# Performance work log

Hardware: AMD Instinct MI355X
Metric: run time of the kernel (lower is better)

Reference implementation:

```python
import jax, jax.numpy as jnp
import numpy as np
import math

B, TSRC, TTGT, DM, DI, H = 2, 2048, 2048, 1024, 1024, 16
DH = DI // H
LN_EPS = 1e-5


def setup_inputs() -> dict:
    key = jax.random.key(0)
    ks = iter(jax.random.split(key, 40))
    def p(*shape):
        return jax.random.normal(next(ks), shape, jnp.float32) * 0.02
    inp = {
        "enc_out_vecs": jax.random.normal(next(ks), (B, TSRC, DM), jnp.float32),
        "output_vecs": jax.random.normal(next(ks), (B, TTGT, DM), jnp.float32),
    }
    for tag in ("dd", "ed"):
        inp["Wq_" + tag] = p(DM, DI); inp["bq_" + tag] = jnp.zeros((DI,), jnp.float32)
        inp["Wk_" + tag] = p(DM, DI); inp["bk_" + tag] = jnp.zeros((DI,), jnp.float32)
        inp["Wv_" + tag] = p(DM, DI); inp["bv_" + tag] = jnp.zeros((DI,), jnp.float32)
        inp["Wo_" + tag] = p(DI, DM); inp["bo_" + tag] = jnp.zeros((DM,), jnp.float32)
        inp["W1_" + tag] = p(DM, 2 * DM); inp["b1_" + tag] = jnp.zeros((2 * DM,), jnp.float32)
        inp["W2_" + tag] = p(2 * DM, DM); inp["b2_" + tag] = jnp.zeros((DM,), jnp.float32)
        inp["g1_" + tag] = jnp.ones((DM,), jnp.float32); inp["be1_" + tag] = jnp.zeros((DM,), jnp.float32)
        inp["g2_" + tag] = jnp.ones((DM,), jnp.float32); inp["be2_" + tag] = jnp.zeros((DM,), jnp.float32)
    return inp


def _ln(x, g, b):
    m = jnp.mean(x, axis=-1, keepdims=True)
    v = jnp.var(x, axis=-1, keepdims=True)
    return (x - m) * jax.lax.rsqrt(v + LN_EPS) * g + b


def _mha(xq, xkv, Wq, bq, Wk, bk, Wv, bv, causal):
    Bb, Tq, _ = xq.shape
    Tk = xkv.shape[1]
    q = (xq @ Wq + bq).reshape(Bb, Tq, H, DH)
    k = (xkv @ Wk + bk).reshape(Bb, Tk, H, DH)
    v = (xkv @ Wv + bv).reshape(Bb, Tk, H, DH)
    s = jnp.einsum("bqhd,bkhd->bhqk", q, k) / math.sqrt(DH)
    if causal:
        mask = jnp.where(jnp.arange(Tk)[None, :] > jnp.arange(Tq)[:, None], -jnp.inf, 0.0)
        s = s + mask
    w = jax.nn.softmax(s, axis=-1)
    return jnp.einsum("bhqk,bkhd->bqhd", w, v).reshape(Bb, Tq, H * DH)


def reference(enc_out_vecs, output_vecs,
              Wq_dd, bq_dd, Wk_dd, bk_dd, Wv_dd, bv_dd, Wo_dd, bo_dd,
              W1_dd, b1_dd, W2_dd, b2_dd, g1_dd, be1_dd, g2_dd, be2_dd,
              Wq_ed, bq_ed, Wk_ed, bk_ed, Wv_ed, bv_ed, Wo_ed, bo_ed,
              W1_ed, b1_ed, W2_ed, b2_ed, g1_ed, be1_ed, g2_ed, be2_ed):
    # masked self-attention over decoder inputs
    x = output_vecs
    a = _mha(x, x, Wq_dd, bq_dd, Wk_dd, bk_dd, Wv_dd, bv_dd, causal=True)
    x = _ln(a @ Wo_dd + bo_dd + x, g1_dd, be1_dd)
    x = _ln(x + jax.nn.relu(x @ W1_dd + b1_dd) @ W2_dd + b2_dd, g2_dd, be2_dd)
    # cross attention against encoder outputs
    a = _mha(x, enc_out_vecs, Wq_ed, bq_ed, Wk_ed, bk_ed, Wv_ed, bv_ed, causal=False)
    x = _ln(a @ Wo_ed + bo_ed + x, g1_ed, be1_ed)
    x = _ln(jax.nn.relu(x @ W1_ed + b1_ed) @ W2_ed + b2_ed + x, g2_ed, be2_ed)
    return x
```

## Files before the change

kernel.cpp:

```cpp
#include <hip/hip_runtime.h>
#include <stdint.h>

#define DEV __device__ __forceinline__
typedef unsigned short u16;
typedef __attribute__((ext_vector_type(8))) short bf16x8;
typedef __attribute__((ext_vector_type(4))) float f32x4;

#define AS1 __attribute__((address_space(1)))
#define AS3 __attribute__((address_space(3)))
#define WAITVM0 asm volatile("s_waitcnt vmcnt(0)" ::: "memory")
#define QSCALE 0.18033688011112042f

DEV u16 f2bf(float f) {
  union { float f; uint32_t u; } x; x.f = f;
  uint32_t r = x.u + 0x7fffu + ((x.u >> 16) & 1u);
  return (u16)(r >> 16);
}

DEV uint32_t cvt_pk_bf16(float a, float b) {
  uint32_t r;
  asm("v_cvt_pk_bf16_f32 %0, %1, %2" : "=v"(r) : "v"(a), "v"(b));
  return r;
}

__global__ __launch_bounds__(256) void k_cvt2(const float* __restrict__ a, const float* __restrict__ bsrc,
                                              u16* __restrict__ oa, u16* __restrict__ ob, int n4) {
  int i = blockIdx.x * blockDim.x + threadIdx.x;
  const float* s;
  u16* o;
  int k;
  if (i < n4) { s = a; o = oa; k = i; }
  else        { s = bsrc; o = ob; k = i - n4; }
  float4 v = reinterpret_cast<const float4*>(s)[k];
  reinterpret_cast<ushort4*>(o)[k] = make_ushort4(f2bf(v.x), f2bf(v.y), f2bf(v.z), f2bf(v.w));
}

struct WTJob { const float* W; u16* WT; int K, M, msh, start; };
struct WTJobs { WTJob j[12]; };

__global__ void k_wT_all(WTJobs jobs) {
  __shared__ float tile[32][33];
  int b = blockIdx.x;
  int i = 0;
#pragma unroll
  for (int t = 1; t < 12; ++t)
    if (b >= jobs.j[t].start) i = t;
  const WTJob J = jobs.j[i];
  int rel = b - J.start;
  int m0 = (rel & ((1 << J.msh) - 1)) << 5;
  int k0 = (rel >> J.msh) << 5;
  int tx = threadIdx.x, ty = threadIdx.y;
#pragma unroll
  for (int q = 0; q < 4; ++q)
    tile[ty + q * 8][tx] = J.W[(size_t)(k0 + ty + q * 8) * J.M + m0 + tx];
  __syncthreads();
#pragma unroll
  for (int q = 0; q < 4; ++q)
    J.WT[(size_t)(m0 + ty + q * 8) * J.K + k0 + tx] = f2bf(tile[tx][ty + q * 8]);
}

template<int R>
DEV void stage_tile(const u16* __restrict__ g, int strideElems, u16* lds, int tid, int wv) {
#pragma unroll
  for (int t = 0; t < R / 32; ++t) {
    int idx = t * 256 + tid;
    int row = idx >> 3;
    int b = (idx & 7) << 4;
    int sb = b ^ ((row & 7) << 4);
    const char* src = (const char*)g + (size_t)row * strideElems * 2 + sb;
    char* dst = (char*)lds + (size_t)(t * 256 + wv * 64) * 16;
    __builtin_amdgcn_global_load_lds((const AS1 void*)src, (AS3 void*)dst, 16, 0, 0);
  }
}

DEV bf16x8 lds_frag(const u16* lds, int row, int kel) {
  int off = row * 128 + ((kel * 2) ^ ((row & 7) << 4));
  return *(const bf16x8*)((const char*)lds + off);
}

template<int MODE>
__global__ __launch_bounds__(256) void k_gemm(const u16* __restrict__ A, int lda,
                                              const u16* __restrict__ BT,
                                              const float* __restrict__ bias,
                                              void* __restrict__ C, int ldc, int K) {
  __shared__ __align__(16) u16 A_lds[2][128 * 64];
  __shared__ __align__(16) u16 B_lds[2][128 * 64];
  const int tid = threadIdx.x, lane = tid & 63, wv = tid >> 6;
  const int wm = wv >> 1, wn = wv & 1;
  const int bm0 = blockIdx.y * 128, bn0 = blockIdx.x * 128;
  const int lr = lane & 15, lk = (lane >> 4) * 8, r0 = (lane >> 4) * 4;

  f32x4 acc[4][4];
#pragma unroll
  for (int i = 0; i < 4; ++i)
#pragma unroll
    for (int j = 0; j < 4; ++j) acc[i][j] = f32x4{0.f, 0.f, 0.f, 0.f};

  stage_tile<128>(A + (size_t)bm0 * lda, lda, A_lds[0], tid, wv);
  stage_tile<128>(BT + (size_t)bn0 * K, K, B_lds[0], tid, wv);
  WAITVM0;
  __builtin_amdgcn_s_barrier();

  int cur = 0;
  for (int k0 = 0; k0 < K; k0 += 64) {
    if (k0 + 64 < K) {
      stage_tile<128>(A + (size_t)bm0 * lda + k0 + 64, lda, A_lds[cur ^ 1], tid, wv);
      stage_tile<128>(BT + (size_t)bn0 * K + k0 + 64, K, B_lds[cur ^ 1], tid, wv);
    }
#pragma unroll
    for (int kk = 0; kk < 2; ++kk) {
      bf16x8 af[4], bfr[4];
#pragma unroll
      for (int i = 0; i < 4; ++i) af[i] = lds_frag(A_lds[cur], wm * 64 + i * 16 + lr, kk * 32 + lk);
#pragma unroll
      for (int j = 0; j < 4; ++j) bfr[j] = lds_frag(B_lds[cur], wn * 64 + j * 16 + lr, kk * 32 + lk);
#pragma unroll
      for (int i = 0; i < 4; ++i)
#pragma unroll
        for (int j = 0; j < 4; ++j)
          acc[i][j] = __builtin_amdgcn_mfma_f32_16x16x32_bf16(af[i], bfr[j], acc[i][j], 0, 0, 0);
    }
    WAITVM0;
    __builtin_amdgcn_s_barrier();
    cur ^= 1;
  }

#pragma unroll
  for (int j = 0; j < 4; ++j) {
    int col = bn0 + wn * 64 + j * 16 + lr;
    float bv = bias[col];
#pragma unroll
    for (int i = 0; i < 4; ++i) {
      int rowb = bm0 + wm * 64 + i * 16 + r0;
      if constexpr (MODE == 0) {
#pragma unroll
        for (int r = 0; r < 4; ++r)
          ((float*)C)[(size_t)(rowb + r) * ldc + col] = acc[i][j][r] + bv;
      } else {
#pragma unroll
        for (int r = 0; r < 4; ++r) {
          float v = fmaxf(acc[i][j][r] + bv, 0.f);
          ((u16*)C)[(size_t)(rowb + r) * ldc + col] = f2bf(v);
        }
      }
    }
  }
}

__global__ __launch_bounds__(256) void k_qkv(const u16* __restrict__ Aq, const u16* __restrict__ Akv,
                                             const u16* __restrict__ BT,
                                             const float* __restrict__ bq, const float* __restrict__ bk,
                                             const float* __restrict__ bv,
                                             u16* __restrict__ Qb, u16* __restrict__ Kb,
                                             u16* __restrict__ Vt, int K) {
  __shared__ __align__(16) u16 A_lds[2][128 * 64];
  __shared__ __align__(16) u16 B_lds[2][128 * 64];
  const int tid = threadIdx.x, lane = tid & 63, wv = tid >> 6;
  const int wm = wv >> 1, wn = wv & 1;
  const int bm0 = blockIdx.y * 128, bn0 = blockIdx.x * 128;
  const int seg = bn0 >> 10;
  const u16* A = (seg == 0) ? Aq : Akv;
  const int lr = lane & 15, lk = (lane >> 4) * 8, r0 = (lane >> 4) * 4;

  f32x4 acc[4][4];
#pragma unroll
  for (int i = 0; i < 4; ++i)
#pragma unroll
    for (int j = 0; j < 4; ++j) acc[i][j] = f32x4{0.f, 0.f, 0.f, 0.f};

  stage_tile<128>(A + (size_t)bm0 * K, K, A_lds[0], tid, wv);
  stage_tile<128>(BT + (size_t)bn0 * K, K, B_lds[0], tid, wv);
  WAITVM0;
  __builtin_amdgcn_s_barrier();

  int cur = 0;
  for (int k0 = 0; k0 < K; k0 += 64) {
    if (k0 + 64 < K) {
      stage_tile<128>(A + (size_t)bm0 * K + k0 + 64, K, A_lds[cur ^ 1], tid, wv);
      stage_tile<128>(BT + (size_t)bn0 * K + k0 + 64, K, B_lds[cur ^ 1], tid, wv);
    }
#pragma unroll
    for (int kk = 0; kk < 2; ++kk) {
      bf16x8 af[4], bfr[4];
#pragma unroll
      for (int i = 0; i < 4; ++i) af[i] = lds_frag(A_lds[cur], wm * 64 + i * 16 + lr, kk * 32 + lk);
#pragma unroll
      for (int j = 0; j < 4; ++j) bfr[j] = lds_frag(B_lds[cur], wn * 64 + j * 16 + lr, kk * 32 + lk);
#pragma unroll
      for (int i = 0; i < 4; ++i)
#pragma unroll
        for (int j = 0; j < 4; ++j)
          acc[i][j] = __builtin_amdgcn_mfma_f32_16x16x32_bf16(af[i], bfr[j], acc[i][j], 0, 0, 0);
    }
    WAITVM0;
    __builtin_amdgcn_s_barrier();
    cur ^= 1;
  }

#pragma unroll
  for (int j = 0; j < 4; ++j) {
    int col = bn0 + wn * 64 + j * 16 + lr;
    int cl = col & 1023;
#pragma unroll
    for (int i = 0; i < 4; ++i) {
      int rowb = bm0 + wm * 64 + i * 16 + r0;
      if (seg == 0) {
        float bb = bq[cl];
#pragma unroll
        for (int r = 0; r < 4; ++r)
          Qb[(size_t)(rowb + r) * 1024 + cl] = f2bf((acc[i][j][r] + bb) * QSCALE);
      } else if (seg == 1) {
        float bb = bk[cl];
#pragma unroll
        for (int r = 0; r < 4; ++r)
          Kb[(size_t)(rowb + r) * 1024 + cl] = f2bf(acc[i][j][r] + bb);
      } else {
        float bb = bv[cl];
        int bidx = rowb >> 11, t = rowb & 2047;
        ushort4 o = make_ushort4(f2bf(acc[i][j][0] + bb), f2bf(acc[i][j][1] + bb),
                                 f2bf(acc[i][j][2] + bb), f2bf(acc[i][j][3] + bb));
        *reinterpret_cast<ushort4*>(&Vt[((size_t)bidx * 1024 + cl) * 2048 + t]) = o;
      }
    }
  }
}

__global__ __launch_bounds__(256) void k_ln(const float* __restrict__ Rm, const float* __restrict__ X,
                                            const float* __restrict__ g, const float* __restrict__ be,
                                            float* __restrict__ Y, u16* __restrict__ Yb) {
  int row = blockIdx.x;
  size_t base4 = (size_t)row * 256;
  int t = threadIdx.x;
  float4 a = reinterpret_cast<const float4*>(Rm)[base4 + t];
  float4 x = reinterpret_cast<const float4*>(X)[base4 + t];
  float v0 = a.x + x.x, v1 = a.y + x.y, v2 = a.z + x.z, v3 = a.w + x.w;
  float s = v0 + v1 + v2 + v3;
  float ss = v0 * v0 + v1 * v1 + v2 * v2 + v3 * v3;
#pragma unroll
  for (int m = 1; m < 64; m <<= 1) { s += __shfl_xor(s, m); ss += __shfl_xor(ss, m); }
  __shared__ float red[8];
  int wv = t >> 6;
  if ((t & 63) == 0) { red[wv] = s; red[4 + wv] = ss; }
  __syncthreads();
  s = red[0] + red[1] + red[2] + red[3];
  ss = red[4] + red[5] + red[6] + red[7];
  float mean = s * (1.f / 1024.f);
  float var = ss * (1.f / 1024.f) - mean * mean;
  float rstd = rsqrtf(var + 1e-5f);
  float4 gv = reinterpret_cast<const float4*>(g)[t];
  float4 bv = reinterpret_cast<const float4*>(be)[t];
  float o0 = (v0 - mean) * rstd * gv.x + bv.x;
  float o1 = (v1 - mean) * rstd * gv.y + bv.y;
  float o2 = (v2 - mean) * rstd * gv.z + bv.z;
  float o3 = (v3 - mean) * rstd * gv.w + bv.w;
  reinterpret_cast<float4*>(Y)[base4 + t] = make_float4(o0, o1, o2, o3);
  if (Yb) {
    ushort4 ob = make_ushort4(f2bf(o0), f2bf(o1), f2bf(o2), f2bf(o3));
    reinterpret_cast<ushort4*>(Yb)[base4 + t] = ob;
  }
}

template<bool CAUSAL>
__global__ __launch_bounds__(256) void k_attn(const u16* __restrict__ Q, const u16* __restrict__ Kg,
                                              const u16* __restrict__ Vt, u16* __restrict__ O, int T) {
  __shared__ __align__(16) u16 K_lds[2][64 * 64];
  __shared__ __align__(16) u16 V_lds[2][64 * 64];
  __shared__ __align__(16) u16 p_lds[4][16 * 64];
  const int tid = threadIdx.x, lane = tid & 63, wv = tid >> 6;
  const int h = blockIdx.y, b = blockIdx.z;
  const int qx = CAUSAL ? (gridDim.x - 1 - blockIdx.x) : blockIdx.x;
  const int q0 = qx * 64;
  const int qw = q0 + wv * 16;
  const int lq = lane & 15, g = lane >> 4;
  const int swz = (lq & 7) << 4;
  const int fb0 = lq * 128 + ((g * 16) ^ swz);
  const int fb1 = lq * 128 + ((g * 16 + 64) ^ swz);
  const size_t qkbase = ((size_t)b * T) * 1024 + h * 64;
  const size_t vbase = ((size_t)b * 1024 + h * 64) * T;

  bf16x8 aq0, aq1;
  {
    const u16* qp = Q + qkbase + (size_t)(qw + lq) * 1024 + g * 8;
    aq0 = *reinterpret_cast<const bf16x8*>(qp);
    aq1 = *reinterpret_cast<const bf16x8*>(qp + 32);
  }

  const int srow = tid >> 3;
  const int ssb = ((tid & 7) << 4) ^ ((srow & 7) << 4);
  const char* ksrc = (const char*)(Kg + qkbase) + (size_t)srow * 2048 + ssb;
  const char* vsrc = (const char*)(Vt + vbase) + (size_t)srow * ((size_t)T * 2) + ssb;
  const int vstep2 = T * 64;
  const uint32_t doff = (uint32_t)((tid & 192) << 4);

  auto stage = [&](const char* kp, const char* vp, int buf) {
    char* kd = (char*)K_lds[buf] + doff;
    char* vd = (char*)V_lds[buf] + doff;
    __builtin_amdgcn_global_load_lds((const AS1 void*)kp, (AS3 void*)kd, 16, 0, 0);
    __builtin_amdgcn_global_load_lds((const AS1 void*)(kp + 65536), (AS3 void*)(kd + 4096), 16, 0, 0);
    __builtin_amdgcn_global_load_lds((const AS1 void*)vp, (AS3 void*)vd, 16, 0, 0);
    __builtin_amdgcn_global_load_lds((const AS1 void*)(vp + vstep2), (AS3 void*)(vd + 4096), 16, 0, 0);
  };

  f32x4 acc[4];
#pragma unroll
  for (int j = 0; j < 4; ++j) acc[j] = f32x4{0.f, 0.f, 0.f, 0.f};
  float lsum = 0.f;

  const int nt = CAUSAL ? (qx + 1) : (T >> 6);

  stage(ksrc, vsrc, 0);
  WAITVM0;
  __builtin_amdgcn_s_barrier();
  ksrc += 131072;
  vsrc += 128;

  char* pw = (char*)p_lds[wv];
  int cur = 0;
  for (int it = 0; it < nt; ++it) {
    const int kv0 = it << 6;
    if (it + 1 < nt) {
      stage(ksrc, vsrc, cur ^ 1);
      ksrc += 131072;
      vsrc += 128;
    }
    const char* kb = (const char*)K_lds[cur];
    const char* vb = (const char*)V_lds[cur];
    f32x4 st[4];
    __builtin_amdgcn_s_setprio(1);
#pragma unroll
    for (int j = 0; j < 4; ++j) {
      bf16x8 bk0 = *reinterpret_cast<const bf16x8*>(kb + fb0 + j * 2048);
      bf16x8 bk1 = *reinterpret_cast<const bf16x8*>(kb + fb1 + j * 2048);
      f32x4 t0 = f32x4{0.f, 0.f, 0.f, 0.f};
      t0 = __builtin_amdgcn_mfma_f32_16x16x32_bf16(bk0, aq0, t0, 0, 0, 0);
      t0 = __builtin_amdgcn_mfma_f32_16x16x32_bf16(bk1, aq1, t0, 0, 0, 0);
      st[j] = t0;
    }
    __builtin_amdgcn_s_setprio(0);
    uint32_t pk[8];
    if (CAUSAL && it == nt - 1) {
      const int qrow = qw + lq;
#pragma unroll
      for (int j = 0; j < 4; ++j) {
        float p0 = __builtin_exp2f(st[j][0]);
        float p1 = __builtin_exp2f(st[j][1]);
        float p2 = __builtin_exp2f(st[j][2]);
        float p3 = __builtin_exp2f(st[j][3]);
        int kvb = kv0 + j * 16 + g * 4;
        p0 = (kvb > qrow) ? 0.f : p0;
        p1 = (kvb + 1 > qrow) ? 0.f : p1;
        p2 = (kvb + 2 > qrow) ? 0.f : p2;
        p3 = (kvb + 3 > qrow) ? 0.f : p3;
        lsum += (p0 + p1) + (p2 + p3);
        pk[2 * j] = cvt_pk_bf16(p0, p1);
        pk[2 * j + 1] = cvt_pk_bf16(p2, p3);
      }
    } else {
#pragma unroll
      for (int j = 0; j < 4; ++j) {
        float p0 = __builtin_exp2f(st[j][0]);
        float p1 = __builtin_exp2f(st[j][1]);
        float p2 = __builtin_exp2f(st[j][2]);
        float p3 = __builtin_exp2f(st[j][3]);
        lsum += (p0 + p1) + (p2 + p3);
        pk[2 * j] = cvt_pk_bf16(p0, p1);
        pk[2 * j + 1] = cvt_pk_bf16(p2, p3);
      }
    }
#pragma unroll
    for (int j = 0; j < 4; ++j)
      *reinterpret_cast<uint2*>(pw + lq * 128 + ((j * 32 + g * 8) ^ swz)) =
          make_uint2(pk[2 * j], pk[2 * j + 1]);
    bf16x8 pf0 = *reinterpret_cast<const bf16x8*>(pw + fb0);
    bf16x8 pf1 = *reinterpret_cast<const bf16x8*>(pw + fb1);
    __builtin_amdgcn_s_setprio(1);
#pragma unroll
    for (int j2 = 0; j2 < 4; ++j2) {
      bf16x8 v0 = *reinterpret_cast<const bf16x8*>(vb + fb0 + j2 * 2048);
      bf16x8 v1 = *reinterpret_cast<const bf16x8*>(vb + fb1 + j2 * 2048);
      acc[j2] = __builtin_amdgcn_mfma_f32_16x16x32_bf16(v0, pf0, acc[j2], 0, 0, 0);
      acc[j2] = __builtin_amdgcn_mfma_f32_16x16x32_bf16(v1, pf1, acc[j2], 0, 0, 0);
    }
    __builtin_amdgcn_s_setprio(0);
    WAITVM0;
    __builtin_amdgcn_s_barrier();
    cur ^= 1;
  }

  lsum += __shfl_xor(lsum, 16);
  lsum += __shfl_xor(lsum, 32);
  float inv = 1.f / lsum;
  size_t rb = qkbase + (size_t)(qw + lq) * 1024;
#pragma unroll
  for (int j2 = 0; j2 < 4; ++j2) {
    ushort4 o = make_ushort4(f2bf(acc[j2][0] * inv), f2bf(acc[j2][1] * inv),
                             f2bf(acc[j2][2] * inv), f2bf(acc[j2][3] * inv));
    *reinterpret_cast<ushort4*>(&O[rb + j2 * 16 + g * 4]) = o;
  }
}

extern "C" void kernel_launch(void* const* d_in, const int* in_sizes, int n_in,
                              void* d_out, int out_size, void* d_ws, size_t ws_size,
                              hipStream_t stream) {
  const int T = 2048;
  const float* enc = (const float*)d_in[0];
  const float* outv = (const float*)d_in[1];
  auto F = [&](int i) { return (const float*)d_in[i]; };

  size_t off = 0;
  auto alloc = [&](size_t bytes) {
    void* p = (char*)d_ws + off;
    off += (bytes + 255) & ~(size_t)255;
    return p;
  };

  const int tdK[12] = {1024, 1024, 1024, 1024, 1024, 2048, 1024, 1024, 1024, 1024, 1024, 2048};
  const int tdM[12] = {1024, 1024, 1024, 1024, 2048, 1024, 1024, 1024, 1024, 1024, 2048, 1024};
  const int tdIdx[12] = {2, 4, 6, 8, 10, 12, 18, 20, 22, 24, 26, 28};
  u16* WT_[12];
  for (int i = 0; i < 12; ++i) WT_[i] = (u16*)alloc((size_t)tdK[i] * tdM[i] * 2);

  u16* Xb0 = (u16*)alloc(4096ull * 1024 * 2);
  u16* Eb = (u16*)alloc(4096ull * 1024 * 2);
  u16* Qb = (u16*)alloc(4096ull * 1024 * 2);
  u16* Kb = (u16*)alloc(4096ull * 1024 * 2);
  u16* Vt = (u16*)alloc(4096ull * 1024 * 2);
  u16* Ab = (u16*)alloc(4096ull * 1024 * 2);
  u16* Hb = (u16*)alloc(4096ull * 2048 * 2);
  u16* Xbc = (u16*)alloc(4096ull * 1024 * 2);
  float* Rf = (float*)alloc(4096ull * 1024 * 4);
  float* Xfa = (float*)alloc(4096ull * 1024 * 4);
  float* Xfb = (float*)alloc(4096ull * 1024 * 4);

  k_cvt2<<<8192, 256, 0, stream>>>(outv, enc, Xb0, Eb, 4096 * 1024 / 4);

  WTJobs jobs;
  int start = 0;
  for (int i = 0; i < 12; ++i) {
    int msh = (tdM[i] == 2048) ? 6 : 5;
    jobs.j[i] = {F(tdIdx[i]), WT_[i], tdK[i], tdM[i], msh, start};
    start += (tdM[i] >> 5) * (tdK[i] >> 5);
  }
  k_wT_all<<<start, dim3(32, 8), 0, stream>>>(jobs);

  dim3 gq(24, 32);
  dim3 g1k(8, 32);
  dim3 g2k(16, 32);
  dim3 ga(32, 16, 2);

  k_qkv<<<gq, 256, 0, stream>>>(Xb0, Xb0, WT_[0], F(3), F(5), F(7), Qb, Kb, Vt, 1024);
  k_attn<true><<<ga, 256, 0, stream>>>(Qb, Kb, Vt, Ab, T);
  k_gemm<0><<<g1k, 256, 0, stream>>>(Ab, 1024, WT_[3], F(9), Rf, 1024, 1024);
  k_ln<<<4096, 256, 0, stream>>>(Rf, outv, F(14), F(15), Xfa, Xbc);
  k_gemm<2><<<g2k, 256, 0, stream>>>(Xbc, 1024, WT_[4], F(11), Hb, 2048, 1024);
  k_gemm<0><<<g1k, 256, 0, stream>>>(Hb, 2048, WT_[5], F(13), Rf, 1024, 2048);
  k_ln<<<4096, 256, 0, stream>>>(Rf, Xfa, F(16), F(17), Xfb, Xbc);

  k_qkv<<<gq, 256, 0, stream>>>(Xbc, Eb, WT_[6], F(19), F(21), F(23), Qb, Kb, Vt, 1024);
  k_attn<false><<<ga, 256, 0, stream>>>(Qb, Kb, Vt, Ab, T);
  k_gemm<0><<<g1k, 256, 0, stream>>>(Ab, 1024, WT_[9], F(25), Rf, 1024, 1024);
  k_ln<<<4096, 256, 0, stream>>>(Rf, Xfb, F(30), F(31), Xfa, Xbc);
  k_gemm<2><<<g2k, 256, 0, stream>>>(Xbc, 1024, WT_[10], F(27), Hb, 2048, 1024);
  k_gemm<0><<<g1k, 256, 0, stream>>>(Hb, 2048, WT_[11], F(29), Rf, 1024, 2048);
  k_ln<<<4096, 256, 0, stream>>>(Rf, Xfa, F(32), F(33), (float*)d_out, (u16*)nullptr);
}
```

Before: 486.1 us.

## Split causal attention KV range across two blocks, shrink GEMM N-tiles, swizzle blocks

Causal self-attention now splits each query tile's KV range into two halves handled by separate blocks. Each block writes unnormalised fp32 partial outputs and row sums, and a new merge kernel combines them into bf16. This balances the triangular workload and doubles the block count. The N=1024 GEMMs and the QKV projection use narrower 64-column tiles for more workgroups, and all GEMMs use a grid swizzle for L2 locality. The cost is extra partial-result traffic, one more launch, and lower per-block arithmetic intensity.

Measured after the change: 452.1 us. 7.0% less time.

```diff
diff --git a/kernel.cpp b/kernel.cpp
--- a/kernel.cpp
+++ b/kernel.cpp
@@ -78,26 +78,31 @@
   return *(const bf16x8*)((const char*)lds + off);
 }
 
-template<int MODE>
+template<int JT, int MODE>
 __global__ __launch_bounds__(256) void k_gemm(const u16* __restrict__ A, int lda,
                                               const u16* __restrict__ BT,
                                               const float* __restrict__ bias,
                                               void* __restrict__ C, int ldc, int K) {
+  constexpr int BN = JT * 32;
   __shared__ __align__(16) u16 A_lds[2][128 * 64];
-  __shared__ __align__(16) u16 B_lds[2][128 * 64];
+  __shared__ __align__(16) u16 B_lds[2][BN * 64];
   const int tid = threadIdx.x, lane = tid & 63, wv = tid >> 6;
   const int wm = wv >> 1, wn = wv & 1;
-  const int bm0 = blockIdx.y * 128, bn0 = blockIdx.x * 128;
+  const int nwg = gridDim.x * gridDim.y;
+  const int flat = blockIdx.y * gridDim.x + blockIdx.x;
+  const int sw = (flat & 7) * (nwg >> 3) + (flat >> 3);
+  const int bx = sw % gridDim.x, by = sw / gridDim.x;
+  const int bm0 = by * 128, bn0 = bx * BN;
   const int lr = lane & 15, lk = (lane >> 4) * 8, r0 = (lane >> 4) * 4;
 
-  f32x4 acc[4][4];
+  f32x4 acc[4][JT];
 #pragma unroll
   for (int i = 0; i < 4; ++i)
 #pragma unroll
-    for (int j = 0; j < 4; ++j) acc[i][j] = f32x4{0.f, 0.f, 0.f, 0.f};
+    for (int j = 0; j < JT; ++j) acc[i][j] = f32x4{0.f, 0.f, 0.f, 0.f};
 
   stage_tile<128>(A + (size_t)bm0 * lda, lda, A_lds[0], tid, wv);
-  stage_tile<128>(BT + (size_t)bn0 * K, K, B_lds[0], tid, wv);
+  stage_tile<BN>(BT + (size_t)bn0 * K, K, B_lds[0], tid, wv);
   WAITVM0;
   __builtin_amdgcn_s_barrier();
 
@@ -105,19 +110,19 @@
   for (int k0 = 0; k0 < K; k0 += 64) {
     if (k0 + 64 < K) {
       stage_tile<128>(A + (size_t)bm0 * lda + k0 + 64, lda, A_lds[cur ^ 1], tid, wv);
-      stage_tile<128>(BT + (size_t)bn0 * K + k0 + 64, K, B_lds[cur ^ 1], tid, wv);
+      stage_tile<BN>(BT + (size_t)bn0 * K + k0 + 64, K, B_lds[cur ^ 1], tid, wv);
     }
 #pragma unroll
     for (int kk = 0; kk < 2; ++kk) {
-      bf16x8 af[4], bfr[4];
+      bf16x8 af[4], bfr[JT];
 #pragma unroll
       for (int i = 0; i < 4; ++i) af[i] = lds_frag(A_lds[cur], wm * 64 + i * 16 + lr, kk * 32 + lk);
 #pragma unroll
-      for (int j = 0; j < 4; ++j) bfr[j] = lds_frag(B_lds[cur], wn * 64 + j * 16 + lr, kk * 32 + lk);
+      for (int j = 0; j < JT; ++j) bfr[j] = lds_frag(B_lds[cur], wn * (JT * 16) + j * 16 + lr, kk * 32 + lk);
 #pragma unroll
       for (int i = 0; i < 4; ++i)
 #pragma unroll
-        for (int j = 0; j < 4; ++j)
+        for (int j = 0; j < JT; ++j)
           acc[i][j] = __builtin_amdgcn_mfma_f32_16x16x32_bf16(af[i], bfr[j], acc[i][j], 0, 0, 0);
     }
     WAITVM0;
@@ -126,8 +131,8 @@
   }
 
 #pragma unroll
-  for (int j = 0; j < 4; ++j) {
-    int col = bn0 + wn * 64 + j * 16 + lr;
+  for (int j = 0; j < JT; ++j) {
+    int col = bn0 + wn * (JT * 16) + j * 16 + lr;
     float bv = bias[col];
 #pragma unroll
     for (int i = 0; i < 4; ++i) {
@@ -154,22 +159,26 @@
                                              u16* __restrict__ Qb, u16* __restrict__ Kb,
                                              u16* __restrict__ Vt, int K) {
   __shared__ __align__(16) u16 A_lds[2][128 * 64];
-  __shared__ __align__(16) u16 B_lds[2][128 * 64];
+  __shared__ __align__(16) u16 B_lds[2][64 * 64];
   const int tid = threadIdx.x, lane = tid & 63, wv = tid >> 6;
   const int wm = wv >> 1, wn = wv & 1;
-  const int bm0 = blockIdx.y * 128, bn0 = blockIdx.x * 128;
+  const int nwg = gridDim.x * gridDim.y;
+  const int flat = blockIdx.y * gridDim.x + blockIdx.x;
+  const int sw = (flat & 7) * (nwg >> 3) + (flat >> 3);
+  const int bx = sw % gridDim.x, by = sw / gridDim.x;
+  const int bm0 = by * 128, bn0 = bx * 64;
   const int seg = bn0 >> 10;
   const u16* A = (seg == 0) ? Aq : Akv;
   const int lr = lane & 15, lk = (lane >> 4) * 8, r0 = (lane >> 4) * 4;
 
-  f32x4 acc[4][4];
+  f32x4 acc[4][2];
 #pragma unroll
   for (int i = 0; i < 4; ++i)
 #pragma unroll
-    for (int j = 0; j < 4; ++j) acc[i][j] = f32x4{0.f, 0.f, 0.f, 0.f};
+    for (int j = 0; j < 2; ++j) acc[i][j] = f32x4{0.f, 0.f, 0.f, 0.f};
 
   stage_tile<128>(A + (size_t)bm0 * K, K, A_lds[0], tid, wv);
-  stage_tile<128>(BT + (size_t)bn0 * K, K, B_lds[0], tid, wv);
+  stage_tile<64>(BT + (size_t)bn0 * K, K, B_lds[0], tid, wv);
   WAITVM0;
   __builtin_amdgcn_s_barrier();
 
@@ -177,19 +186,19 @@
   for (int k0 = 0; k0 < K; k0 += 64) {
     if (k0 + 64 < K) {
       stage_tile<128>(A + (size_t)bm0 * K + k0 + 64, K, A_lds[cur ^ 1], tid, wv);
-      stage_tile<128>(BT + (size_t)bn0 * K + k0 + 64, K, B_lds[cur ^ 1], tid, wv);
+      stage_tile<64>(BT + (size_t)bn0 * K + k0 + 64, K, B_lds[cur ^ 1], tid, wv);
     }
 #pragma unroll
     for (int kk = 0; kk < 2; ++kk) {
-      bf16x8 af[4], bfr[4];
+      bf16x8 af[4], bfr[2];
 #pragma unroll
       for (int i = 0; i < 4; ++i) af[i] = lds_frag(A_lds[cur], wm * 64 + i * 16 + lr, kk * 32 + lk);
 #pragma unroll
-      for (int j = 0; j < 4; ++j) bfr[j] = lds_frag(B_lds[cur], wn * 64 + j * 16 + lr, kk * 32 + lk);
+      for (int j = 0; j < 2; ++j) bfr[j] = lds_frag(B_lds[cur], wn * 32 + j * 16 + lr, kk * 32 + lk);
 #pragma unroll
       for (int i = 0; i < 4; ++i)
 #pragma unroll
-        for (int j = 0; j < 4; ++j)
+        for (int j = 0; j < 2; ++j)
           acc[i][j] = __builtin_amdgcn_mfma_f32_16x16x32_bf16(af[i], bfr[j], acc[i][j], 0, 0, 0);
     }
     WAITVM0;
@@ -198,8 +207,8 @@
   }
 
 #pragma unroll
-  for (int j = 0; j < 4; ++j) {
-    int col = bn0 + wn * 64 + j * 16 + lr;
+  for (int j = 0; j < 2; ++j) {
+    int col = bn0 + wn * 32 + j * 16 + lr;
     int cl = col & 1023;
 #pragma unroll
     for (int i = 0; i < 4; ++i) {
@@ -262,15 +271,14 @@
 
 template<bool CAUSAL>
 __global__ __launch_bounds__(256) void k_attn(const u16* __restrict__ Q, const u16* __restrict__ Kg,
-                                              const u16* __restrict__ Vt, u16* __restrict__ O, int T) {
+                                              const u16* __restrict__ Vt, u16* __restrict__ O,
+                                              float* __restrict__ OP0, float* __restrict__ OP1,
+                                              float* __restrict__ L0, float* __restrict__ L1, int T) {
   __shared__ __align__(16) u16 K_lds[2][64 * 64];
   __shared__ __align__(16) u16 V_lds[2][64 * 64];
   __shared__ __align__(16) u16 p_lds[4][16 * 64];
   const int tid = threadIdx.x, lane = tid & 63, wv = tid >> 6;
   const int h = blockIdx.y, b = blockIdx.z;
-  const int qx = CAUSAL ? (gridDim.x - 1 - blockIdx.x) : blockIdx.x;
-  const int q0 = qx * 64;
-  const int qw = q0 + wv * 16;
   const int lq = lane & 15, g = lane >> 4;
   const int swz = (lq & 7) << 4;
   const int fb0 = lq * 128 + ((g * 16) ^ swz);
@@ -278,17 +286,32 @@
   const size_t qkbase = ((size_t)b * T) * 1024 + h * 64;
   const size_t vbase = ((size_t)b * 1024 + h * 64) * T;
 
+  int qx, st, en;
+  if constexpr (CAUSAL) {
+    qx = 31 - (blockIdx.x >> 1);
+    const int s = blockIdx.x & 1;
+    const int ntf = qx + 1, half = (ntf + 1) >> 1;
+    st = s ? half : 0;
+    en = s ? ntf : half;
+  } else {
+    qx = blockIdx.x;
+    st = 0;
+    en = T >> 6;
+  }
+  const int nt = en - st;
+  const int qw = qx * 64 + wv * 16;
+
   bf16x8 aq0, aq1;
   {
-    const u16* qp = Q + qkbase + (size_t)(qw + lq) * 1024 + g * 8;
-    aq0 = *reinterpret_cast<const bf16x8*>(qp);
-    aq1 = *reinterpret_cast<const bf16x8*>(qp + 32);
+    const u16* qp_ = Q + qkbase + (size_t)(qw + lq) * 1024 + g * 8;
+    aq0 = *reinterpret_cast<const bf16x8*>(qp_);
+    aq1 = *reinterpret_cast<const bf16x8*>(qp_ + 32);
   }
 
   const int srow = tid >> 3;
   const int ssb = ((tid & 7) << 4) ^ ((srow & 7) << 4);
-  const char* ksrc = (const char*)(Kg + qkbase) + (size_t)srow * 2048 + ssb;
-  const char* vsrc = (const char*)(Vt + vbase) + (size_t)srow * ((size_t)T * 2) + ssb;
+  const char* ksrc = (const char*)(Kg + qkbase) + (size_t)srow * 2048 + ssb + (size_t)st * 131072;
+  const char* vsrc = (const char*)(Vt + vbase) + (size_t)srow * ((size_t)T * 2) + ssb + (size_t)st * 128;
   const int vstep2 = T * 64;
   const uint32_t doff = (uint32_t)((tid & 192) << 4);
 
@@ -302,101 +325,127 @@
   };
 
   f32x4 acc[4];
+  float lsum = 0.f;
 #pragma unroll
   for (int j = 0; j < 4; ++j) acc[j] = f32x4{0.f, 0.f, 0.f, 0.f};
-  float lsum = 0.f;
-
-  const int nt = CAUSAL ? (qx + 1) : (T >> 6);
-
-  stage(ksrc, vsrc, 0);
-  WAITVM0;
-  __builtin_amdgcn_s_barrier();
-  ksrc += 131072;
-  vsrc += 128;
 
   char* pw = (char*)p_lds[wv];
-  int cur = 0;
-  for (int it = 0; it < nt; ++it) {
-    const int kv0 = it << 6;
-    if (it + 1 < nt) {
-      stage(ksrc, vsrc, cur ^ 1);
-      ksrc += 131072;
-      vsrc += 128;
-    }
-    const char* kb = (const char*)K_lds[cur];
-    const char* vb = (const char*)V_lds[cur];
-    f32x4 st[4];
-    __builtin_amdgcn_s_setprio(1);
-#pragma unroll
-    for (int j = 0; j < 4; ++j) {
-      bf16x8 bk0 = *reinterpret_cast<const bf16x8*>(kb + fb0 + j * 2048);
-      bf16x8 bk1 = *reinterpret_cast<const bf16x8*>(kb + fb1 + j * 2048);
-      f32x4 t0 = f32x4{0.f, 0.f, 0.f, 0.f};
-      t0 = __builtin_amdgcn_mfma_f32_16x16x32_bf16(bk0, aq0, t0, 0, 0, 0);
-      t0 = __builtin_amdgcn_mfma_f32_16x16x32_bf16(bk1, aq1, t0, 0, 0, 0);
-      st[j] = t0;
-    }
-    __builtin_amdgcn_s_setprio(0);
-    uint32_t pk[8];
-    if (CAUSAL && it == nt - 1) {
-      const int qrow = qw + lq;
-#pragma unroll
-      for (int j = 0; j < 4; ++j) {
-        float p0 = __builtin_exp2f(st[j][0]);
-        float p1 = __builtin_exp2f(st[j][1]);
-        float p2 = __builtin_exp2f(st[j][2]);
-        float p3 = __builtin_exp2f(st[j][3]);
-        int kvb = kv0 + j * 16 + g * 4;
-        p0 = (kvb > qrow) ? 0.f : p0;
-        p1 = (kvb + 1 > qrow) ? 0.f : p1;
-        p2 = (kvb + 2 > qrow) ? 0.f : p2;
-        p3 = (kvb + 3 > qrow) ? 0.f : p3;
-        lsum += (p0 + p1) + (p2 + p3);
-        pk[2 * j] = cvt_pk_bf16(p0, p1);
-        pk[2 * j + 1] = cvt_pk_bf16(p2, p3);
-      }
-    } else {
-#pragma unroll
-      for (int j = 0; j < 4; ++j) {
-        float p0 = __builtin_exp2f(st[j][0]);
-        float p1 = __builtin_exp2f(st[j][1]);
-        float p2 = __builtin_exp2f(st[j][2]);
-        float p3 = __builtin_exp2f(st[j][3]);
-        lsum += (p0 + p1) + (p2 + p3);
-        pk[2 * j] = cvt_pk_bf16(p0, p1);
-        pk[2 * j + 1] = cvt_pk_bf16(p2, p3);
-      }
-    }
-#pragma unroll
-    for (int j = 0; j < 4; ++j)
-      *reinterpret_cast<uint2*>(pw + lq * 128 + ((j * 32 + g * 8) ^ swz)) =
-          make_uint2(pk[2 * j], pk[2 * j + 1]);
-    bf16x8 pf0 = *reinterpret_cast<const bf16x8*>(pw + fb0);
-    bf16x8 pf1 = *reinterpret_cast<const bf16x8*>(pw + fb1);
-    __builtin_amdgcn_s_setprio(1);
-#pragma unroll
-    for (int j2 = 0; j2 < 4; ++j2) {
-      bf16x8 v0 = *reinterpret_cast<const bf16x8*>(vb + fb0 + j2 * 2048);
-      bf16x8 v1 = *reinterpret_cast<const bf16x8*>(vb + fb1 + j2 * 2048);
-      acc[j2] = __builtin_amdgcn_mfma_f32_16x16x32_bf16(v0, pf0, acc[j2], 0, 0, 0);
-      acc[j2] = __builtin_amdgcn_mfma_f32_16x16x32_bf16(v1, pf1, acc[j2], 0, 0, 0);
-    }
-    __builtin_amdgcn_s_setprio(0);
+
+  if (nt > 0) {
+    stage(ksrc, vsrc, 0);
     WAITVM0;
     __builtin_amdgcn_s_barrier();
-    cur ^= 1;
+    ksrc += 131072;
+    vsrc += 128;
+
+    int cur = 0;
+    for (int it = st; it < en; ++it) {
+      if (it + 1 < en) {
+        stage(ksrc, vsrc, cur ^ 1);
+        ksrc += 131072;
+        vsrc += 128;
+      }
+      const char* kb = (const char*)K_lds[cur];
+      const char* vb = (const char*)V_lds[cur];
+      f32x4 st_[4];
+      __builtin_amdgcn_s_setprio(1);
+#pragma unroll
+      for (int j = 0; j < 4; ++j) {
+        bf16x8 bk0 = *reinterpret_cast<const bf16x8*>(kb + fb0 + j * 2048);
+        bf16x8 bk1 = *reinterpret_cast<const bf16x8*>(kb + fb1 + j * 2048);
+        f32x4 t0 = f32x4{0.f, 0.f, 0.f, 0.f};
+        t0 = __builtin_amdgcn_mfma_f32_16x16x32_bf16(bk0, aq0, t0, 0, 0, 0);
+        t0 = __builtin_amdgcn_mfma_f32_16x16x32_bf16(bk1, aq1, t0, 0, 0, 0);
+        st_[j] = t0;
+      }
+      __builtin_amdgcn_s_setprio(0);
+      uint32_t pk[8];
+      if (CAUSAL && it == qx) {
+        const int qrow = qw + lq, kv0 = it << 6;
+#pragma unroll
+        for (int j = 0; j < 4; ++j) {
+          float p0 = __builtin_exp2f(st_[j][0]);
+          float p1 = __builtin_exp2f(st_[j][1]);
+          float p2 = __builtin_exp2f(st_[j][2]);
+          float p3 = __builtin_exp2f(st_[j][3]);
+          int kvb = kv0 + j * 16 + g * 4;
+          p0 = (kvb > qrow) ? 0.f : p0;
+          p1 = (kvb + 1 > qrow) ? 0.f : p1;
+          p2 = (kvb + 2 > qrow) ? 0.f : p2;
+          p3 = (kvb + 3 > qrow) ? 0.f : p3;
+          lsum += (p0 + p1) + (p2 + p3);
+          pk[2 * j] = cvt_pk_bf16(p0, p1);
+          pk[2 * j + 1] = cvt_pk_bf16(p2, p3);
+        }
+      } else {
+#pragma unroll
+        for (int j = 0; j < 4; ++j) {
+          float p0 = __builtin_exp2f(st_[j][0]);
+          float p1 = __builtin_exp2f(st_[j][1]);
+          float p2 = __builtin_exp2f(st_[j][2]);
+          float p3 = __builtin_exp2f(st_[j][3]);
+          lsum += (p0 + p1) + (p2 + p3);
+          pk[2 * j] = cvt_pk_bf16(p0, p1);
+          pk[2 * j + 1] = cvt_pk_bf16(p2, p3);
+        }
+      }
+#pragma unroll
+      for (int j = 0; j < 4; ++j)
+        *reinterpret_cast<uint2*>(pw + lq * 128 + ((j * 32 + g * 8) ^ swz)) =
+            make_uint2(pk[2 * j], pk[2 * j + 1]);
+      bf16x8 pf0 = *reinterpret_cast<const bf16x8*>(pw + fb0);
+      bf16x8 pf1 = *reinterpret_cast<const bf16x8*>(pw + fb1);
+      __builtin_amdgcn_s_setprio(1);
+#pragma unroll
+      for (int j2 = 0; j2 < 4; ++j2) {
+        bf16x8 v0 = *reinterpret_cast<const bf16x8*>(vb + fb0 + j2 * 2048);
+        bf16x8 v1 = *reinterpret_cast<const bf16x8*>(vb + fb1 + j2 * 2048);
+        acc[j2] = __builtin_amdgcn_mfma_f32_16x16x32_bf16(v0, pf0, acc[j2], 0, 0, 0);
+        acc[j2] = __builtin_amdgcn_mfma_f32_16x16x32_bf16(v1, pf1, acc[j2], 0, 0, 0);
+      }
+      __builtin_amdgcn_s_setprio(0);
+      WAITVM0;
+      __builtin_amdgcn_s_barrier();
+      cur ^= 1;
+    }
   }
 
   lsum += __shfl_xor(lsum, 16);
   lsum += __shfl_xor(lsum, 32);
-  float inv = 1.f / lsum;
-  size_t rb = qkbase + (size_t)(qw + lq) * 1024;
-#pragma unroll
-  for (int j2 = 0; j2 < 4; ++j2) {
-    ushort4 o = make_ushort4(f2bf(acc[j2][0] * inv), f2bf(acc[j2][1] * inv),
-                             f2bf(acc[j2][2] * inv), f2bf(acc[j2][3] * inv));
-    *reinterpret_cast<ushort4*>(&O[rb + j2 * 16 + g * 4]) = o;
-  }
+  if constexpr (CAUSAL) {
+    float* OP = (blockIdx.x & 1) ? OP1 : OP0;
+    float* Lp = (blockIdx.x & 1) ? L1 : L0;
+    const int row = (b * 16 + h) * 2048 + qw + lq;
+    float* pr = OP + (size_t)row * 64;
+#pragma unroll
+    for (int j2 = 0; j2 < 4; ++j2)
+      *reinterpret_cast<f32x4*>(pr + j2 * 16 + g * 4) = acc[j2];
+    if (g == 0) Lp[row] = lsum;
+  } else {
+    float inv = 1.f / lsum;
+    size_t rb = qkbase + (size_t)(qw + lq) * 1024;
+#pragma unroll
+    for (int j2 = 0; j2 < 4; ++j2) {
+      ushort4 o = make_ushort4(f2bf(acc[j2][0] * inv), f2bf(acc[j2][1] * inv),
+                               f2bf(acc[j2][2] * inv), f2bf(acc[j2][3] * inv));
+      *reinterpret_cast<ushort4*>(&O[rb + j2 * 16 + g * 4]) = o;
+    }
+  }
+}
+
+__global__ __launch_bounds__(256) void k_amrg(const float* __restrict__ P0, const float* __restrict__ P1,
+                                              const float* __restrict__ L0, const float* __restrict__ L1,
+                                              u16* __restrict__ Ab) {
+  int i = blockIdx.x * 256 + threadIdx.x;
+  int row = i >> 4, d4 = (i & 15) << 2;
+  f32x4 a = *reinterpret_cast<const f32x4*>(&P0[(size_t)row * 64 + d4]);
+  f32x4 c = *reinterpret_cast<const f32x4*>(&P1[(size_t)row * 64 + d4]);
+  float inv = 1.f / (L0[row] + L1[row]);
+  int bh = row >> 11, q = row & 2047, bb = bh >> 4, hh = bh & 15;
+  size_t dst = ((size_t)(bb * 2048 + q)) * 1024 + hh * 64 + d4;
+  ushort4 o = make_ushort4(f2bf((a[0] + c[0]) * inv), f2bf((a[1] + c[1]) * inv),
+                           f2bf((a[2] + c[2]) * inv), f2bf((a[3] + c[3]) * inv));
+  *reinterpret_cast<ushort4*>(&Ab[dst]) = o;
 }
 
 extern "C" void kernel_launch(void* const* d_in, const int* in_sizes, int n_in,
@@ -431,6 +480,7 @@
   float* Rf = (float*)alloc(4096ull * 1024 * 4);
   float* Xfa = (float*)alloc(4096ull * 1024 * 4);
   float* Xfb = (float*)alloc(4096ull * 1024 * 4);
+  float* Lsum = (float*)alloc(2ull * 65536 * 4);
 
   k_cvt2<<<8192, 256, 0, stream>>>(outv, enc, Xb0, Eb, 4096 * 1024 / 4);
 
@@ -443,24 +493,31 @@
   }
   k_wT_all<<<start, dim3(32, 8), 0, stream>>>(jobs);
 
-  dim3 gq(24, 32);
-  dim3 g1k(8, 32);
+  float* OP0 = Rf;
+  float* OP1 = (float*)Hb;
+  float* L0 = Lsum;
+  float* L1 = Lsum + 65536;
+
+  dim3 gq(48, 32);
+  dim3 g1k(16, 32);
   dim3 g2k(16, 32);
-  dim3 ga(32, 16, 2);
+  dim3 gac(64, 16, 2);
+  dim3 gan(32, 16, 2);
 
   k_qkv<<<gq, 256, 0, stream>>>(Xb0, Xb0, WT_[0], F(3), F(5), F(7), Qb, Kb, Vt, 1024);
-  k_attn<true><<<ga, 256, 0, stream>>>(Qb, Kb, Vt, Ab, T);
-  k_gemm<0><<<g1k, 256, 0, stream>>>(Ab, 1024, WT_[3], F(9), Rf, 1024, 1024);
+  k_attn<true><<<gac, 256, 0, stream>>>(Qb, Kb, Vt, Ab, OP0, OP1, L0, L1, T);
+  k_amrg<<<4096, 256, 0, stream>>>(OP0, OP1, L0, L1, Ab);
+  k_gemm<2, 0><<<g1k, 256, 0, stream>>>(Ab, 1024, WT_[3], F(9), Rf, 1024, 1024);
   k_ln<<<4096, 256, 0, stream>>>(Rf, outv, F(14), F(15), Xfa, Xbc);
-  k_gemm<2><<<g2k, 256, 0, stream>>>(Xbc, 1024, WT_[4], F(11), Hb, 2048, 1024);
-  k_gemm<0><<<g1k, 256, 0, stream>>>(Hb, 2048, WT_[5], F(13), Rf, 1024, 2048);
+  k_gemm<4, 2><<<g2k, 256, 0, stream>>>(Xbc, 1024, WT_[4], F(11), Hb, 2048, 1024);
+  k_gemm<2, 0><<<g1k, 256, 0, stream>>>(Hb, 2048, WT_[5], F(13), Rf, 1024, 2048);
   k_ln<<<4096, 256, 0, stream>>>(Rf, Xfa, F(16), F(17), Xfb, Xbc);
 
   k_qkv<<<gq, 256, 0, stream>>>(Xbc, Eb, WT_[6], F(19), F(21), F(23), Qb, Kb, Vt, 1024);
-  k_attn<false><<<ga, 256, 0, stream>>>(Qb, Kb, Vt, Ab, T);
-  k_gemm<0><<<g1k, 256, 0, stream>>>(Ab, 1024, WT_[9], F(25), Rf, 1024, 1024);
+  k_attn<false><<<gan, 256, 0, stream>>>(Qb, Kb, Vt, Ab, OP0, OP1, L0, L1, T);
+  k_gemm<2, 0><<<g1k, 256, 0, stream>>>(Ab, 1024, WT_[9], F(25), Rf, 1024, 1024);
   k_ln<<<4096, 256, 0, stream>>>(Rf, Xfb, F(30), F(31), Xfa, Xbc);
-  k_gemm<2><<<g2k, 256, 0, stream>>>(Xbc, 1024, WT_[10], F(27), Hb, 2048, 1024);
-  k_gemm<0><<<g1k, 256, 0, stream>>>(Hb, 2048, WT_[11], F(29), Rf, 1024, 2048);
+  k_gemm<4, 2><<<g2k, 256, 0, stream>>>(Xbc, 1024, WT_[10], F(27), Hb, 2048, 1024);
+  k_gemm<2, 0><<<g1k, 256, 0, stream>>>(Hb, 2048, WT_[11], F(29), Rf, 1024, 2048);
   k_ln<<<4096, 256, 0, stream>>>(Rf, Xfa, F(32), F(33), (float*)d_out, (u16*)nullptr);
 }
```
